# Kernel tuning notes

Measured on AMD Instinct MI355X. Metric: run time of the kernel, lower is better.

Reference implementation:

```python
import jax, jax.numpy as jnp
import numpy as np

C64 = jnp.complex64
NQ_PER_NEIGHBOR = 4
TOTAL_QUBITS = 16  # (max_neighbors=3 + self) * 4


def rx_matrix(theta):
    h = 0.5 * theta
    c = jnp.cos(h).astype(C64)
    s = (-1j) * jnp.sin(h)
    return jnp.stack([jnp.stack([c, s], -1), jnp.stack([s, c], -1)], -2)


def ry_matrix(theta):
    h = 0.5 * theta
    c, s = jnp.cos(h), jnp.sin(h)
    return jnp.stack([jnp.stack([c, -s], -1), jnp.stack([s, c], -1)], -2).astype(C64)


def rz_matrix(theta):
    em = jnp.exp(-0.5j * theta).astype(C64)
    ep = jnp.exp(0.5j * theta).astype(C64)
    z = jnp.zeros_like(em)
    return jnp.stack([jnp.stack([em, z], -1), jnp.stack([z, ep], -1)], -2)


def zz_diag(theta):
    # diagonal of Ising ZZ gate on |00>,|01>,|10>,|11>
    em = jnp.exp(-0.5j * theta).astype(C64)
    ep = jnp.exp(0.5j * theta).astype(C64)
    return jnp.stack([em, ep, ep, em], -1)  # (..., 4)


def apply_1q(state, gate, q, n):
    # state: (B, 2^n). Equivalent to torch permute+einsum('boi,ij->boj'):
    # contract the target qubit axis with gate[i, j] (note: gate index order as in source).
    B = state.shape[0]
    L, R = 2 ** q, 2 ** (n - 1 - q)
    s = state.reshape(B, L, 2, R)
    if gate.ndim == 2:
        s = jnp.einsum('blir,ij->bljr', s, gate)
    else:  # batched gate (B,2,2)
        s = jnp.einsum('blir,bij->bljr', s, gate)
    return s.reshape(B, 2 ** n)


def apply_zz_adjacent(state, d, q, n):
    # diagonal 2-qubit gate on adjacent qubits (q, q+1); d: (4,)
    B = state.shape[0]
    L, R = 2 ** q, 2 ** (n - q - 2)
    s = state.reshape(B, L, 4, R) * d[None, None, :, None]
    return s.reshape(B, 2 ** n)


def quantum_convolution(state, rot, zz, n):
    d = zz_diag(zz)  # (n-1, 4)
    for i in range(n - 1):
        state = apply_zz_adjacent(state, d[i], i, n)
    rx, ry, rz = rx_matrix(rot[:, 0]), ry_matrix(rot[:, 1]), rz_matrix(rot[:, 2])
    for q in range(n):
        state = apply_1q(state, rx[q], q, n)
        state = apply_1q(state, ry[q], q, n)
        state = apply_1q(state, rz[q], q, n)
    return state


def quantum_pooling(state, n):
    # trace out odd-indexed (0-based) qubits, keep even-indexed
    B = state.shape[0]
    s = state.reshape((B,) + (2,) * n)
    keep = list(range(1, n + 1, 2))
    trace = list(range(2, n + 1, 2))
    s = jnp.transpose(s, [0] + trace + keep)
    nt = len(trace)
    s = s.reshape(B, 2 ** nt, -1)
    probs = jnp.sum(jnp.abs(s) ** 2, axis=-1, keepdims=True)
    probs = probs / (jnp.sum(probs, axis=1, keepdims=True) + 1e-10)
    s = jnp.sum(s * jnp.sqrt(probs), axis=1)
    norm = jnp.sqrt(jnp.sum(jnp.abs(s) ** 2, axis=-1, keepdims=True) + 1e-10)
    return s / norm, len(keep)


def measure_z(state, n):
    probs = jnp.abs(state) ** 2  # (B, 2^n)
    idx = np.arange(2 ** n)
    bits = (idx[None, :] >> (n - 1 - np.arange(n))[:, None]) & 1  # (n, 2^n)
    signs = jnp.asarray(1.0 - 2.0 * bits, jnp.float32)
    return probs @ signs.T  # (B, n)


def setup_inputs() -> dict:
    key = jax.random.key(0)
    ks = jax.random.split(key, 10)
    B, K, D = 64, 3, 128
    return {
        'neighbor_features': jax.random.normal(ks[0], (B, K, D), jnp.float32),
        'self_features': jax.random.normal(ks[1], (B, D), jnp.float32),
        'Wp': jax.random.normal(ks[2], (12, D), jnp.float32) * 0.05,
        'bp': jax.random.normal(ks[3], (12,), jnp.float32) * 0.05,
        'rot0': jax.random.normal(ks[4], (16, 3), jnp.float32) * 0.1,
        'zz0': jax.random.normal(ks[5], (15,), jnp.float32) * 0.1,
        'rot1': jax.random.normal(ks[6], (8, 3), jnp.float32) * 0.1,
        'zz1': jax.random.normal(ks[7], (7,), jnp.float32) * 0.1,
        'Wo': jax.random.normal(ks[8], (64, 4), jnp.float32) * 0.1,
        'bo': jax.random.normal(ks[9], (64,), jnp.float32) * 0.1,
    }


def reference(neighbor_features, self_features, Wp, bp, rot0, zz0, rot1, zz1, Wo, bo):
    B = neighbor_features.shape[0]
    all_f = jnp.concatenate([self_features[:, None, :], neighbor_features], axis=1)  # (B, 4, D)
    angles = (all_f @ Wp.T + bp).reshape(B, TOTAL_QUBITS, 3)  # (B, 16, 3)

    state = jnp.zeros((B, 2 ** TOTAL_QUBITS), C64).at[:, 0].set(1.0)
    rx = rx_matrix(angles[:, :, 0])  # (B, 16, 2, 2)
    ry = ry_matrix(angles[:, :, 1])
    rz = rz_matrix(angles[:, :, 2])
    for q in range(TOTAL_QUBITS):
        state = apply_1q(state, rx[:, q], q, TOTAL_QUBITS)
        state = apply_1q(state, ry[:, q], q, TOTAL_QUBITS)
        state = apply_1q(state, rz[:, q], q, TOTAL_QUBITS)

    n = TOTAL_QUBITS
    for rot, zz in ((rot0, zz0), (rot1, zz1)):
        state = quantum_convolution(state, rot, zz, n)
        state, n = quantum_pooling(state, n)

    z = measure_z(state, n)  # (B, final_qubits=4)
    return z @ Wo.T + bo
```

## Files before the change

### kernel.cpp

```cpp
#include <hip/hip_runtime.h>
#include <math.h>

#define NB 64

struct C { float x, y; };

__device__ __forceinline__ C cmul(C a, C b){ return C{a.x*b.x - a.y*b.y, a.x*b.y + a.y*b.x}; }

__device__ __forceinline__ void bfly(C& x0, C& x1, const C* G){
  C n0 = C{x0.x*G[0].x - x0.y*G[0].y + x1.x*G[2].x - x1.y*G[2].y,
           x0.x*G[0].y + x0.y*G[0].x + x1.x*G[2].y + x1.y*G[2].x};
  C n1 = C{x0.x*G[1].x - x0.y*G[1].y + x1.x*G[3].x - x1.y*G[3].y,
           x0.x*G[1].y + x0.y*G[1].x + x1.x*G[3].y + x1.y*G[3].x};
  x0 = n0; x1 = n1;
}

__device__ __forceinline__ int expand44(int t2, int k2){
  int j=0;
  #pragma unroll
  for (int m=0;m<4;m++){ j |= ((t2>>m)&1)<<(2*m); j |= ((k2>>m)&1)<<(2*m+1); }
  return j;
}

__device__ void fused_M(float tx, float ty, float tz, C* M){
  float cx=cosf(0.5f*tx), sx=sinf(0.5f*tx);
  float cy=cosf(0.5f*ty), sy=sinf(0.5f*ty);
  float cz=cosf(0.5f*tz), sz=sinf(0.5f*tz);
  C b0 = C{ cx*cy, -sx*sy};
  C b1 = C{-cx*sy, -sx*cy};
  C b2 = C{ cx*sy, -sx*cy};
  C b3 = C{ cx*cy,  sx*sy};
  C e0 = C{cz,-sz}, e1 = C{cz, sz};
  M[0]=cmul(b0,e0); M[1]=cmul(b1,e1);
  M[2]=cmul(b2,e0); M[3]=cmul(b3,e1);
}

__global__ __launch_bounds__(256) void k_all(
    const float* __restrict__ nbr, const float* __restrict__ slf,
    const float* __restrict__ Wp, const float* __restrict__ bp,
    const float* __restrict__ rot0, const float* __restrict__ zz0,
    const float* __restrict__ rot1, const float* __restrict__ zz1,
    const float* __restrict__ Wo, const float* __restrict__ bo,
    float* __restrict__ out)
{
  const int b = blockIdx.x, tid = threadIdx.x;

  __shared__ float thp[48][4];
  __shared__ float th[48];
  __shared__ C vq[16][2];
  __shared__ float zz0s[15];
  __shared__ C M0s[16][4];
  __shared__ C lam[2];
  __shared__ C W[4][256];
  __shared__ float GH00[16], GH11[16];
  __shared__ float GL00[16], GL11[16];
  __shared__ C GH01[16], GL01[16];
  __shared__ float w[256], red[256];
  __shared__ C Mx[2][16][16];
  __shared__ C s8[256];
  __shared__ C M1s[8][4];
  __shared__ float zz1s[7];
  __shared__ float p2[16];
  __shared__ C s2[16];
  __shared__ float sc[2];
  __shared__ float zm[4];

  if (tid < 15) zz0s[tid] = zz0[tid];
  if (tid < 192){
    int o = tid>>2, part = tid&3;
    int g = o/12, j = o - g*12;
    const float* f = (g==0) ? (slf + (size_t)b*128) : (nbr + ((size_t)b*3 + (g-1))*128);
    const float4* f4 = (const float4*)(f + part*32);
    const float4* w4 = (const float4*)(Wp + j*128 + part*32);
    float acc = 0.f;
    #pragma unroll
    for (int d=0; d<8; d++){
      float4 a = f4[d], c = w4[d];
      acc += a.x*c.x + a.y*c.y + a.z*c.z + a.w*c.w;
    }
    thp[o][part] = acc;
  }
  __syncthreads();
  if (tid < 48) th[tid] = thp[tid][0]+thp[tid][1]+thp[tid][2]+thp[tid][3] + bp[tid%12];
  if (tid >= 64 && tid < 80){
    int q = tid-64;
    fused_M(rot0[q*3+0], rot0[q*3+1], rot0[q*3+2], &M0s[q][0]);
  }
  if (tid == 80){
    float s,c; sincosf(0.5f*zz0[7],&s,&c);
    lam[0] = C{c,0.f}; lam[1] = C{0.f,-s};
  }
  __syncthreads();
  if (tid < 16){
    C M[4]; fused_M(th[tid*3+0], th[tid*3+1], th[tid*3+2], M);
    vq[tid][0] = M[0]; vq[tid][1] = M[1];
  }
  __syncthreads();

  {
    int h = tid;
    C p = vq[0][(h>>7)&1];
    #pragma unroll
    for (int q=1;q<8;q++) p = cmul(p, vq[q][(h>>(7-q))&1]);
    float A = 0.f;
    #pragma unroll
    for (int kk=0;kk<7;kk++){
      int b0=(h>>(7-kk))&1, b1=(h>>(6-kk))&1;
      A += (b0==b1) ? zz0s[kk] : -zz0s[kk];
    }
    float s,c; sincosf(0.5f*A,&s,&c);
    C Vh = cmul(p, C{c,-s});
    C pl = vq[8][(h>>7)&1];
    #pragma unroll
    for (int q=9;q<16;q++) pl = cmul(pl, vq[q][(h>>(15-q))&1]);
    float Al = 0.f;
    #pragma unroll
    for (int kk=8;kk<15;kk++){
      int b0=(h>>(15-kk))&1, b1=(h>>(14-kk))&1;
      Al += (b0==b1) ? zz0s[kk] : -zz0s[kk];
    }
    sincosf(0.5f*Al,&s,&c);
    C Vl = cmul(pl, C{c,-s});
    W[0][h] = cmul(Vh, lam[0]);
    C a1 = cmul(Vh, lam[1]);
    if (h & 1){ a1.x = -a1.x; a1.y = -a1.y; }
    W[1][h] = a1;
    W[2][h] = Vl;
    W[3][h] = ((h>>7)&1) ? C{-Vl.x,-Vl.y} : Vl;
  }
  __syncthreads();

  for (int pb=0; pb<8; ++pb){
    int arr = tid>>6, pi = tid&63;
    const C* G = (arr<2) ? &M0s[7-pb][0] : &M0s[15-pb][0];
    int m = 1<<pb;
    #pragma unroll
    for (int rep=0; rep<2; ++rep){
      int p = pi + rep*64;
      int x = ((p>>pb)<<(pb+1)) | (p & (m-1));
      C x0 = W[arr][x], x1 = W[arr][x|m];
      bfly(x0,x1,G);
      W[arr][x]=x0; W[arr][x|m]=x1;
    }
    __syncthreads();
  }

  if (tid < 32){
    int side = tid>>4, tq = tid&15;
    float g00=0.f, g11=0.f; C g01{0.f,0.f};
    #pragma unroll
    for (int kq=0;kq<16;kq++){
      int idx = expand44(tq,kq);
      C a0 = W[side*2+0][idx], a1 = W[side*2+1][idx];
      g00 += a0.x*a0.x + a0.y*a0.y;
      g11 += a1.x*a1.x + a1.y*a1.y;
      g01.x += a0.x*a1.x + a0.y*a1.y;
      g01.y += a0.y*a1.x - a0.x*a1.y;
    }
    if (side==0){ GH00[tq]=g00; GH11[tq]=g11; GH01[tq]=g01; }
    else        { GL00[tq]=g00; GL11[tq]=g11; GL01[tq]=g01; }
  }
  __syncthreads();

  {
    int tH = tid>>4, tL = tid&15;
    C gh = GH01[tH], gl = GL01[tL];
    float p = GH00[tH]*GL00[tL] + GH11[tH]*GL11[tL]
            + 2.f*(gh.x*gl.x - gh.y*gl.y);
    p = fmaxf(p, 0.f);
    red[tid] = p; w[tid] = p;
  }
  __syncthreads();
  for (int s=128; s>0; s>>=1){ if (tid<s) red[tid]+=red[tid+s]; __syncthreads(); }
  float tot = red[0];
  __syncthreads();
  w[tid] = sqrtf(w[tid]/(tot + 1e-10f));
  __syncthreads();

  #pragma unroll
  for (int rep=0; rep<2; ++rep){
    int e = tid + rep*256;
    int r = e>>8, tH = (e>>4)&15, kL = e&15;
    C acc{0.f,0.f};
    #pragma unroll
    for (int tL=0;tL<16;tL++){
      float ww = w[(tH<<4)|tL];
      C bv = W[2+r][expand44(tL,kL)];
      acc.x += ww*bv.x; acc.y += ww*bv.y;
    }
    Mx[r][tH][kL] = acc;
  }
  __syncthreads();

  C s1{0.f,0.f};
  {
    int kH = tid>>4, kL = tid&15;
    #pragma unroll
    for (int tH=0;tH<16;tH++){
      int ia = expand44(tH,kH);
      C a0 = W[0][ia], m0 = Mx[0][tH][kL];
      C a1 = W[1][ia], m1 = Mx[1][tH][kL];
      s1.x += a0.x*m0.x - a0.y*m0.y + a1.x*m1.x - a1.y*m1.y;
      s1.y += a0.x*m0.y + a0.y*m0.x + a1.x*m1.y + a1.y*m1.x;
    }
  }
  red[tid] = s1.x*s1.x + s1.y*s1.y;
  __syncthreads();
  for (int s=128; s>0; s>>=1){ if (tid<s) red[tid]+=red[tid+s]; __syncthreads(); }
  float n1 = sqrtf(red[0] + 1e-10f);
  s1.x /= n1; s1.y /= n1;

  if (tid < 8) fused_M(rot1[tid*3+0], rot1[tid*3+1], rot1[tid*3+2], &M1s[tid][0]);
  if (tid >= 8 && tid < 15) zz1s[tid-8] = zz1[tid-8];
  __syncthreads();
  float A = 0.f;
  #pragma unroll
  for (int kk=0;kk<7;kk++){
    int b0=(tid>>(7-kk))&1, b1=(tid>>(6-kk))&1;
    A += (b0==b1) ? zz1s[kk] : -zz1s[kk];
  }
  float sa,ca; sincosf(0.5f*A,&sa,&ca);
  s8[tid] = cmul(s1, C{ca,-sa});
  __syncthreads();
  for (int q=0;q<8;q++){
    int p = 7-q, m = 1<<p;
    if ((tid & m) == 0){
      C x0=s8[tid], x1=s8[tid|m];
      bfly(x0,x1,&M1s[q][0]);
      s8[tid]=x0; s8[tid|m]=x1;
    }
    __syncthreads();
  }
  if (tid < 16){
    float s = 0.f;
    #pragma unroll
    for (int k2=0;k2<16;k2++){ C v=s8[expand44(tid,k2)]; s += v.x*v.x + v.y*v.y; }
    p2[tid] = s;
  }
  __syncthreads();
  if (tid == 0){ float S2=0.f; for (int i2=0;i2<16;i2++) S2+=p2[i2]; sc[0]=S2; }
  __syncthreads();
  if (tid < 16) p2[tid] = sqrtf(p2[tid]/(sc[0]+1e-10f));
  __syncthreads();
  if (tid < 16){
    C a2 = C{0.f,0.f};
    #pragma unroll
    for (int t2=0;t2<16;t2++){ C v=s8[expand44(t2,tid)]; float ww=p2[t2]; a2.x+=v.x*ww; a2.y+=v.y*ww; }
    s2[tid] = a2;
  }
  __syncthreads();
  if (tid == 0){
    float nn=0.f; for (int i2=0;i2<16;i2++) nn += s2[i2].x*s2[i2].x + s2[i2].y*s2[i2].y;
    sc[1] = nn + 1e-10f;
  }
  __syncthreads();
  if (tid < 4){
    float z = 0.f;
    #pragma unroll
    for (int idx=0; idx<16; idx++){
      C v = s2[idx];
      float pr = (v.x*v.x + v.y*v.y)/sc[1];
      z += ((idx>>(3-tid))&1) ? -pr : pr;
    }
    zm[tid] = z;
  }
  __syncthreads();
  if (tid < 64){
    float r = bo[tid];
    #pragma unroll
    for (int q=0;q<4;q++) r += zm[q]*Wo[tid*4+q];
    out[(size_t)b*64 + tid] = r;
  }
}

extern "C" void kernel_launch(void* const* d_in, const int* in_sizes, int n_in,
                              void* d_out, int out_size, void* d_ws, size_t ws_size,
                              hipStream_t stream) {
  const float* nbr  = (const float*)d_in[0];
  const float* slf  = (const float*)d_in[1];
  const float* Wp   = (const float*)d_in[2];
  const float* bp   = (const float*)d_in[3];
  const float* rot0 = (const float*)d_in[4];
  const float* zz0  = (const float*)d_in[5];
  const float* rot1 = (const float*)d_in[6];
  const float* zz1  = (const float*)d_in[7];
  const float* Wo   = (const float*)d_in[8];
  const float* bo   = (const float*)d_in[9];
  float* out = (float*)d_out;

  hipLaunchKernelGGL(k_all, dim3(NB), dim3(256), 0, stream,
                     nbr, slf, Wp, bp, rot0, zz0, rot1, zz1, Wo, bo, out);
}
```

Baseline: 20.18 us.

## Cut block barriers via wave shuffles, radix-4 butterflies, and hoisted parameter setup

Replaces the shared-memory tree reductions with 64-lane wave shuffle reductions plus a 4-entry partial array. Butterfly passes are merged two qubits at a time (radix-4), which halves the number of barrier-separated stages. The final pooling and measurement tail now runs inside a single wave using shuffles instead of several single-thread phases with syncs. Setup of the rot1 and zz1 parameters and the Wo/bo loads is moved into otherwise idle threads at the start, so their latency is hidden. The kernel is latency- and barrier-bound, and the change trades barriers for shuffle work and more register use.

```diff
diff --git a/kernel.cpp b/kernel.cpp
--- a/kernel.cpp
+++ b/kernel.cpp
@@ -52,44 +52,46 @@
   __shared__ C M0s[16][4];
   __shared__ C lam[2];
   __shared__ C W[4][256];
-  __shared__ float GH00[16], GH11[16];
-  __shared__ float GL00[16], GL11[16];
+  __shared__ float GH00[16], GH11[16], GL00[16], GL11[16];
   __shared__ C GH01[16], GL01[16];
-  __shared__ float w[256], red[256];
+  __shared__ float w[256];
+  __shared__ float part[4];
   __shared__ C Mx[2][16][16];
   __shared__ C s8[256];
   __shared__ C M1s[8][4];
   __shared__ float zz1s[7];
-  __shared__ float p2[16];
-  __shared__ C s2[16];
-  __shared__ float sc[2];
-  __shared__ float zm[4];
+
+  float4 wo4 = make_float4(0.f,0.f,0.f,0.f); float bor = 0.f;
+  if (tid < 64){ wo4 = ((const float4*)Wo)[tid]; bor = bo[tid]; }
 
   if (tid < 15) zz0s[tid] = zz0[tid];
   if (tid < 192){
-    int o = tid>>2, part = tid&3;
+    int o = tid>>2, prt = tid&3;
     int g = o/12, j = o - g*12;
     const float* f = (g==0) ? (slf + (size_t)b*128) : (nbr + ((size_t)b*3 + (g-1))*128);
-    const float4* f4 = (const float4*)(f + part*32);
-    const float4* w4 = (const float4*)(Wp + j*128 + part*32);
+    const float4* f4 = (const float4*)(f + prt*32);
+    const float4* w4 = (const float4*)(Wp + j*128 + prt*32);
     float acc = 0.f;
     #pragma unroll
     for (int d=0; d<8; d++){
       float4 a = f4[d], c = w4[d];
       acc += a.x*c.x + a.y*c.y + a.z*c.z + a.w*c.w;
     }
-    thp[o][part] = acc;
-  }
-  __syncthreads();
-  if (tid < 48) th[tid] = thp[tid][0]+thp[tid][1]+thp[tid][2]+thp[tid][3] + bp[tid%12];
-  if (tid >= 64 && tid < 80){
-    int q = tid-64;
+    thp[o][prt] = acc;
+  } else if (tid < 208){
+    int q = tid-192;
     fused_M(rot0[q*3+0], rot0[q*3+1], rot0[q*3+2], &M0s[q][0]);
-  }
-  if (tid == 80){
+  } else if (tid < 216){
+    int q = tid-208;
+    fused_M(rot1[q*3+0], rot1[q*3+1], rot1[q*3+2], &M1s[q][0]);
+  } else if (tid < 223){
+    zz1s[tid-216] = zz1[tid-216];
+  } else if (tid == 223){
     float s,c; sincosf(0.5f*zz0[7],&s,&c);
     lam[0] = C{c,0.f}; lam[1] = C{0.f,-s};
   }
+  __syncthreads();
+  if (tid < 48) th[tid] = thp[tid][0]+thp[tid][1]+thp[tid][2]+thp[tid][3] + bp[tid%12];
   __syncthreads();
   if (tid < 16){
     C M[4]; fused_M(th[tid*3+0], th[tid*3+1], th[tid*3+2], M);
@@ -130,18 +132,17 @@
   }
   __syncthreads();
 
-  for (int pb=0; pb<8; ++pb){
-    int arr = tid>>6, pi = tid&63;
-    const C* G = (arr<2) ? &M0s[7-pb][0] : &M0s[15-pb][0];
-    int m = 1<<pb;
-    #pragma unroll
-    for (int rep=0; rep<2; ++rep){
-      int p = pi + rep*64;
-      int x = ((p>>pb)<<(pb+1)) | (p & (m-1));
-      C x0 = W[arr][x], x1 = W[arr][x|m];
-      bfly(x0,x1,G);
-      W[arr][x]=x0; W[arr][x|m]=x1;
-    }
+  #pragma unroll
+  for (int p=0; p<8; p+=2){
+    int arr = tid>>6, i = tid&63;
+    const C* Glo = (arr<2) ? &M0s[7-p][0]  : &M0s[15-p][0];
+    const C* Ghi = (arr<2) ? &M0s[6-p][0]  : &M0s[14-p][0];
+    int mp = 1<<p;
+    int x = ((i>>p)<<(p+2)) | (i & (mp-1));
+    C c0 = W[arr][x], c1 = W[arr][x|mp], c2 = W[arr][x|(mp<<1)], c3 = W[arr][x|mp|(mp<<1)];
+    bfly(c0,c1,Glo); bfly(c2,c3,Glo);
+    bfly(c0,c2,Ghi); bfly(c1,c3,Ghi);
+    W[arr][x]=c0; W[arr][x|mp]=c1; W[arr][x|(mp<<1)]=c2; W[arr][x|mp|(mp<<1)]=c3;
     __syncthreads();
   }
 
@@ -162,19 +163,24 @@
   }
   __syncthreads();
 
+  float pv;
   {
     int tH = tid>>4, tL = tid&15;
     C gh = GH01[tH], gl = GL01[tL];
-    float p = GH00[tH]*GL00[tL] + GH11[tH]*GL11[tL]
-            + 2.f*(gh.x*gl.x - gh.y*gl.y);
-    p = fmaxf(p, 0.f);
-    red[tid] = p; w[tid] = p;
-  }
-  __syncthreads();
-  for (int s=128; s>0; s>>=1){ if (tid<s) red[tid]+=red[tid+s]; __syncthreads(); }
-  float tot = red[0];
-  __syncthreads();
-  w[tid] = sqrtf(w[tid]/(tot + 1e-10f));
+    pv = GH00[tH]*GL00[tL] + GH11[tH]*GL11[tL] + 2.f*(gh.x*gl.x - gh.y*gl.y);
+    pv = fmaxf(pv, 0.f);
+  }
+  {
+    float v = pv;
+    #pragma unroll
+    for (int off=32; off>0; off>>=1) v += __shfl_down(v, off);
+    if ((tid&63)==0) part[tid>>6] = v;
+  }
+  __syncthreads();
+  {
+    float tot = part[0]+part[1]+part[2]+part[3];
+    w[tid] = sqrtf(pv/(tot + 1e-10f));
+  }
   __syncthreads();
 
   #pragma unroll
@@ -204,71 +210,75 @@
       s1.y += a0.x*m0.y + a0.y*m0.x + a1.x*m1.y + a1.y*m1.x;
     }
   }
-  red[tid] = s1.x*s1.x + s1.y*s1.y;
-  __syncthreads();
-  for (int s=128; s>0; s>>=1){ if (tid<s) red[tid]+=red[tid+s]; __syncthreads(); }
-  float n1 = sqrtf(red[0] + 1e-10f);
-  s1.x /= n1; s1.y /= n1;
-
-  if (tid < 8) fused_M(rot1[tid*3+0], rot1[tid*3+1], rot1[tid*3+2], &M1s[tid][0]);
-  if (tid >= 8 && tid < 15) zz1s[tid-8] = zz1[tid-8];
-  __syncthreads();
-  float A = 0.f;
+  {
+    float v = s1.x*s1.x + s1.y*s1.y;
+    #pragma unroll
+    for (int off=32; off>0; off>>=1) v += __shfl_down(v, off);
+    if ((tid&63)==0) part[tid>>6] = v;
+  }
+  __syncthreads();
+  {
+    float n1 = sqrtf(part[0]+part[1]+part[2]+part[3] + 1e-10f);
+    s1.x /= n1; s1.y /= n1;
+  }
+  {
+    float A = 0.f;
+    #pragma unroll
+    for (int kk=0;kk<7;kk++){
+      int b0=(tid>>(7-kk))&1, b1=(tid>>(6-kk))&1;
+      A += (b0==b1) ? zz1s[kk] : -zz1s[kk];
+    }
+    float sa,ca; sincosf(0.5f*A,&sa,&ca);
+    s8[tid] = cmul(s1, C{ca,-sa});
+  }
+  __syncthreads();
+
   #pragma unroll
-  for (int kk=0;kk<7;kk++){
-    int b0=(tid>>(7-kk))&1, b1=(tid>>(6-kk))&1;
-    A += (b0==b1) ? zz1s[kk] : -zz1s[kk];
-  }
-  float sa,ca; sincosf(0.5f*A,&sa,&ca);
-  s8[tid] = cmul(s1, C{ca,-sa});
-  __syncthreads();
-  for (int q=0;q<8;q++){
-    int p = 7-q, m = 1<<p;
-    if ((tid & m) == 0){
-      C x0=s8[tid], x1=s8[tid|m];
-      bfly(x0,x1,&M1s[q][0]);
-      s8[tid]=x0; s8[tid|m]=x1;
+  for (int j=0; j<4; ++j){
+    if (tid < 64){
+      int hb = 7-2*j, lb = 6-2*j;
+      int ml = 1<<lb, mh = 1<<hb;
+      int x = ((tid>>lb)<<(lb+1)) | (tid & (ml-1));
+      x = ((x>>hb)<<(hb+1)) | (x & (mh-1));
+      C c0 = s8[x], c1 = s8[x|mh], c2 = s8[x|ml], c3 = s8[x|mh|ml];
+      bfly(c0,c1,&M1s[2*j][0]);   bfly(c2,c3,&M1s[2*j][0]);
+      bfly(c0,c2,&M1s[2*j+1][0]); bfly(c1,c3,&M1s[2*j+1][0]);
+      s8[x]=c0; s8[x|mh]=c1; s8[x|ml]=c2; s8[x|mh|ml]=c3;
     }
     __syncthreads();
   }
-  if (tid < 16){
-    float s = 0.f;
-    #pragma unroll
-    for (int k2=0;k2<16;k2++){ C v=s8[expand44(tid,k2)]; s += v.x*v.x + v.y*v.y; }
-    p2[tid] = s;
-  }
-  __syncthreads();
-  if (tid == 0){ float S2=0.f; for (int i2=0;i2<16;i2++) S2+=p2[i2]; sc[0]=S2; }
-  __syncthreads();
-  if (tid < 16) p2[tid] = sqrtf(p2[tid]/(sc[0]+1e-10f));
-  __syncthreads();
-  if (tid < 16){
-    C a2 = C{0.f,0.f};
-    #pragma unroll
-    for (int t2=0;t2<16;t2++){ C v=s8[expand44(t2,tid)]; float ww=p2[t2]; a2.x+=v.x*ww; a2.y+=v.y*ww; }
-    s2[tid] = a2;
-  }
-  __syncthreads();
-  if (tid == 0){
-    float nn=0.f; for (int i2=0;i2<16;i2++) nn += s2[i2].x*s2[i2].x + s2[i2].y*s2[i2].y;
-    sc[1] = nn + 1e-10f;
-  }
-  __syncthreads();
-  if (tid < 4){
-    float z = 0.f;
+
+  if (tid < 64){
+    int ld = tid & 15;
+    float p2v = 0.f;
+    #pragma unroll
+    for (int k2=0;k2<16;k2++){ C v=s8[expand44(ld,k2)]; p2v += v.x*v.x + v.y*v.y; }
+    float S2 = p2v;
+    #pragma unroll
+    for (int off=1; off<16; off<<=1) S2 += __shfl_xor(S2, off);
+    float w2 = sqrtf(p2v/(S2 + 1e-10f));
+    C a2{0.f,0.f};
+    #pragma unroll
+    for (int t2=0;t2<16;t2++){
+      float ww = __shfl(w2, t2);
+      C v = s8[expand44(t2, ld)];
+      a2.x += v.x*ww; a2.y += v.y*ww;
+    }
+    float nn = a2.x*a2.x + a2.y*a2.y;
+    #pragma unroll
+    for (int off=1; off<16; off<<=1) nn += __shfl_xor(nn, off);
+    nn += 1e-10f;
+    float pr = (a2.x*a2.x + a2.y*a2.y)/nn;
+    float z0=0.f,z1=0.f,z2=0.f,z3=0.f;
     #pragma unroll
     for (int idx=0; idx<16; idx++){
-      C v = s2[idx];
-      float pr = (v.x*v.x + v.y*v.y)/sc[1];
-      z += ((idx>>(3-tid))&1) ? -pr : pr;
-    }
-    zm[tid] = z;
-  }
-  __syncthreads();
-  if (tid < 64){
-    float r = bo[tid];
-    #pragma unroll
-    for (int q=0;q<4;q++) r += zm[q]*Wo[tid*4+q];
+      float p_ = __shfl(pr, idx);
+      z0 += ((idx>>3)&1) ? -p_ : p_;
+      z1 += ((idx>>2)&1) ? -p_ : p_;
+      z2 += ((idx>>1)&1) ? -p_ : p_;
+      z3 += ( idx     &1) ? -p_ : p_;
+    }
+    float r = bor + z0*wo4.x + z1*wo4.y + z2*wo4.z + z3*wo4.w;
     out[(size_t)b*64 + tid] = r;
   }
 }
```

After: 17.50 us, median of 2. 1.15x faster.
